# Optimization experiments

Measured on AMD Instinct MI355X. Metric: run time of the kernel, lower is better.

The kernel has to match this reference:

```python
import jax, jax.numpy as jnp
import numpy as np

N_HEADS = 8
N_GROUPS = 8  # n_channels=256 > 64
COLOR_WEIGHT = 1.2
EPS = 1e-5


def setup_inputs() -> dict:
    key = jax.random.key(0)
    ks = jax.random.split(key, 6)
    B, C, H, W = 16, 256, 32, 32
    x = jax.random.normal(ks[0], (B, C, H, W), dtype=jnp.float32)
    std = 0.02
    wq = jax.random.normal(ks[1], (C, C), dtype=jnp.float32) * std
    wk = jax.random.normal(ks[2], (C, C), dtype=jnp.float32) * std
    wv = jax.random.normal(ks[3], (C, C), dtype=jnp.float32) * std
    wo = jax.random.normal(ks[4], (C, C), dtype=jnp.float32) * std
    bq = jnp.zeros((C,), jnp.float32)
    bk = jnp.zeros((C,), jnp.float32)
    bv = jnp.zeros((C,), jnp.float32)
    bo = jnp.zeros((C,), jnp.float32)
    gn_w = jnp.ones((C,), jnp.float32)
    gn_b = jnp.zeros((C,), jnp.float32)
    return {"x": x, "wq": wq, "bq": bq, "wk": wk, "bk": bk,
            "wv": wv, "bv": bv, "wo": wo, "bo": bo,
            "gn_w": gn_w, "gn_b": gn_b}


def reference(x, wq, bq, wk, bk, wv, bv, wo, bo, gn_w, gn_b):
    B, C, H, W = x.shape
    S = H * W
    nh = N_HEADS
    hd = C // nh
    scale = hd ** (-0.5)

    # GroupNorm over (channels_per_group, spatial) per sample
    xf = x.reshape(B, C, S)
    xg = xf.reshape(B, N_GROUPS, (C // N_GROUPS) * S)
    mean = xg.mean(axis=-1, keepdims=True)
    var = xg.var(axis=-1, keepdims=True)
    xn = ((xg - mean) * jax.lax.rsqrt(var + EPS)).reshape(B, C, S)
    xn = xn * gn_w[None, :, None] + gn_b[None, :, None]

    xt = jnp.swapaxes(xn, 1, 2)  # [B, S, C]
    q = xt @ wq.T + bq
    k = xt @ wk.T + bk
    v = xt @ wv.T + bv
    # [B, S, C] -> [B, nh, S, hd]
    q = q.reshape(B, S, nh, hd).transpose(0, 2, 1, 3)
    k = k.reshape(B, S, nh, hd).transpose(0, 2, 1, 3)
    v = v.reshape(B, S, nh, hd).transpose(0, 2, 1, 3)

    attn = jnp.einsum('bhid,bhjd->bhij', q, k) * scale  # [B, nh, S, S]
    # color bias (is_grayscale=False path): k.transpose(-2,-1).reshape(B,nh,S,hd)
    k_color = jnp.swapaxes(k, -2, -1).reshape(B, nh, S, hd)
    color_attn = jnp.abs(q - k_color).mean(axis=-1, keepdims=True)  # [B,nh,S,1]
    attn = attn + COLOR_WEIGHT * color_attn
    attn = jax.nn.softmax(attn, axis=-1)
    # dropout is inference no-op

    out = jnp.einsum('bhij,bhjd->bhid', attn, v)  # [B, nh, S, hd]
    out = out.transpose(0, 2, 1, 3).reshape(B, S, C)
    out = out @ wo.T + bo
    out = jnp.swapaxes(out, 1, 2).reshape(B, C, H, W)
    return out
```

## Files before the change

### kernel.cpp

```cpp
#include <hip/hip_runtime.h>


typedef __attribute__((ext_vector_type(8))) short bf16x8;
typedef __attribute__((ext_vector_type(4))) float f32x4;

static __device__ __forceinline__ unsigned cvt_pk(float lo, float hi) {
  unsigned r;
  asm("v_cvt_pk_bf16_f32 %0, %1, %2" : "=v"(r) : "v"(lo), "v"(hi));
  return r;
}

__global__ __launch_bounds__(256) void prep_kernel(
    const float* __restrict__ x, float2* __restrict__ stats,
    const float* __restrict__ w0, const float* __restrict__ w1,
    const float* __restrict__ w2, const float* __restrict__ w3,
    short* __restrict__ o0, short* __restrict__ o1,
    short* __restrict__ o2, short* __restrict__ o3) {
  int tid = threadIdx.x;
  if (blockIdx.x < 128) {
    __shared__ float red[8];
    int bg = blockIdx.x;
    const float4* x4 = (const float4*)(x + (size_t)bg * 32 * 1024);
    float s = 0.f, ss = 0.f;
    for (int i = tid; i < 8192; i += 256) {
      float4 vv = x4[i];
      s += (vv.x + vv.y) + (vv.z + vv.w);
      ss += vv.x * vv.x + vv.y * vv.y + vv.z * vv.z + vv.w * vv.w;
    }
#pragma unroll
    for (int o = 32; o > 0; o >>= 1) {
      s += __shfl_down(s, o);
      ss += __shfl_down(ss, o);
    }
    if ((tid & 63) == 0) { red[tid >> 6] = s; red[4 + (tid >> 6)] = ss; }
    __syncthreads();
    if (tid == 0) {
      float S = (red[0] + red[1]) + (red[2] + red[3]);
      float SS = (red[4] + red[5]) + (red[6] + red[7]);
      float mean = S * (1.f / 32768.f);
      float var = SS * (1.f / 32768.f) - mean * mean;
      stats[bg] = make_float2(mean, rsqrtf(var + 1e-5f));
    }
  } else {
    int idx = blockIdx.x - 128;
    int sel = idx >> 5, blk = idx & 31;
    const float* src = sel == 0 ? w0 : sel == 1 ? w1 : sel == 2 ? w2 : w3;
    short* dst = sel == 0 ? o0 : sel == 1 ? o1 : sel == 2 ? o2 : o3;
    int i = (blk * 256 + tid) * 8;
    float4 a = *(const float4*)(src + i);
    float4 b = *(const float4*)(src + i + 4);
    uint4 r;
    r.x = cvt_pk(a.x, a.y);
    r.y = cvt_pk(a.z, a.w);
    r.z = cvt_pk(b.x, b.y);
    r.w = cvt_pk(b.z, b.w);
    *(uint4*)(dst + i) = r;
  }
}

__global__ __launch_bounds__(256, 4) void qkv_mfma(
    const float* __restrict__ x, const float2* __restrict__ stats,
    const float* __restrict__ gnw, const float* __restrict__ gnb,
    const short* __restrict__ Wq, const short* __restrict__ Wk,
    const short* __restrict__ Wv,
    const float* __restrict__ bq, const float* __restrict__ bk,
    const float* __restrict__ bv, short* __restrict__ outq,
    short* __restrict__ outk, short* __restrict__ outvt, float scaleq) {
  __shared__ __align__(16) char smem[20480];
  short* As = (short*)smem;
  int tid = threadIdx.x;
  int m0 = blockIdx.x * 64, n0 = blockIdx.y * 64;
  int w = tid >> 6, lane = tid & 63, g = lane >> 4, c = lane & 15;
  int wm = w >> 1, wn = w & 1;
  int srow = tid >> 2, sk = (tid & 3) * 8;
  int bsmp = m0 >> 10, s0 = m0 & 1023;
  int c2 = tid & 15, sg = tid >> 4;
  const float4* xb = (const float4*)(x + (size_t)(bsmp * 256) * 1024);
  unsigned* A32 = (unsigned*)As;
  f32x4 accq[2][2], acck[2][2], accv[2][2];
#pragma unroll
  for (int i = 0; i < 2; ++i)
#pragma unroll
    for (int j = 0; j < 2; ++j) {
      accq[i][j] = (f32x4){0.f, 0.f, 0.f, 0.f};
      acck[i][j] = (f32x4){0.f, 0.f, 0.f, 0.f};
      accv[i][j] = (f32x4){0.f, 0.f, 0.f, 0.f};
    }
  for (int kb = 0; kb < 8; ++kb) {
    float2 st = stats[bsmp * 8 + kb];
    int ch0 = kb * 32 + c2 * 2;
    float a0 = gnw[ch0] * st.y, b0v = gnb[ch0] - st.x * a0;
    float a1 = gnw[ch0 + 1] * st.y, b1v = gnb[ch0 + 1] - st.x * a1;
    float4 u = xb[(size_t)ch0 * 256 + (s0 >> 2) + sg];
    float4 v = xb[(size_t)(ch0 + 1) * 256 + (s0 >> 2) + sg];
    __syncthreads();
    {
      int r0 = (sg * 4) * 20 + c2;
      A32[r0]      = cvt_pk(u.x * a0 + b0v, v.x * a1 + b1v);
      A32[r0 + 20] = cvt_pk(u.y * a0 + b0v, v.y * a1 + b1v);
      A32[r0 + 40] = cvt_pk(u.z * a0 + b0v, v.z * a1 + b1v);
      A32[r0 + 60] = cvt_pk(u.w * a0 + b0v, v.w * a1 + b1v);
    }
    *(bf16x8*)(As + 2560 + srow * 40 + sk) =
        *(const bf16x8*)(Wq + (size_t)(n0 + srow) * 256 + kb * 32 + sk);
    *(bf16x8*)(As + 5120 + srow * 40 + sk) =
        *(const bf16x8*)(Wk + (size_t)(n0 + srow) * 256 + kb * 32 + sk);
    *(bf16x8*)(As + 7680 + srow * 40 + sk) =
        *(const bf16x8*)(Wv + (size_t)(n0 + srow) * 256 + kb * 32 + sk);
    __syncthreads();
    bf16x8 af[2], wfq[2], wfk[2], wfv[2];
#pragma unroll
    for (int i = 0; i < 2; ++i)
      af[i] = *(const bf16x8*)(As + (wm * 32 + i * 16 + c) * 40 + g * 8);
#pragma unroll
    for (int j = 0; j < 2; ++j) {
      int rr = (wn * 32 + j * 16 + c) * 40 + g * 8;
      wfq[j] = *(const bf16x8*)(As + 2560 + rr);
      wfk[j] = *(const bf16x8*)(As + 5120 + rr);
      wfv[j] = *(const bf16x8*)(As + 7680 + rr);
    }
#pragma unroll
    for (int i = 0; i < 2; ++i)
#pragma unroll
      for (int j = 0; j < 2; ++j) {
        accq[i][j] = __builtin_amdgcn_mfma_f32_16x16x32_bf16(wfq[j], af[i], accq[i][j], 0, 0, 0);
        acck[i][j] = __builtin_amdgcn_mfma_f32_16x16x32_bf16(wfk[j], af[i], acck[i][j], 0, 0, 0);
        accv[i][j] = __builtin_amdgcn_mfma_f32_16x16x32_bf16(af[i], wfv[j], accv[i][j], 0, 0, 0);
      }
  }
  __syncthreads();
  short* Tb = (short*)smem;
  int mrd = tid >> 2, ncol = (tid & 3) * 16;
#pragma unroll
  for (int i = 0; i < 2; ++i)
#pragma unroll
    for (int j = 0; j < 2; ++j) {
      float4 b4 = *(const float4*)&bq[n0 + wn * 32 + j * 16 + 4 * g];
      float v0 = (accq[i][j][0] + b4.x) * scaleq;
      float v1 = (accq[i][j][1] + b4.y) * scaleq;
      float v2 = (accq[i][j][2] + b4.z) * scaleq;
      float v3 = (accq[i][j][3] + b4.w) * scaleq;
      *(uint2*)(Tb + (wm * 32 + i * 16 + c) * 72 + wn * 32 + j * 16 + 4 * g) =
          make_uint2(cvt_pk(v0, v1), cvt_pk(v2, v3));
    }
  __syncthreads();
  {
    bf16x8 r0 = *(const bf16x8*)(Tb + mrd * 72 + ncol);
    bf16x8 r1 = *(const bf16x8*)(Tb + mrd * 72 + ncol + 8);
    short* dst = outq + (size_t)(m0 + mrd) * 256 + n0 + ncol;
    *(bf16x8*)dst = r0;
    *(bf16x8*)(dst + 8) = r1;
  }
  __syncthreads();
#pragma unroll
  for (int i = 0; i < 2; ++i)
#pragma unroll
    for (int j = 0; j < 2; ++j) {
      float4 b4 = *(const float4*)&bk[n0 + wn * 32 + j * 16 + 4 * g];
      float v0 = acck[i][j][0] + b4.x;
      float v1 = acck[i][j][1] + b4.y;
      float v2 = acck[i][j][2] + b4.z;
      float v3 = acck[i][j][3] + b4.w;
      *(uint2*)(Tb + (wm * 32 + i * 16 + c) * 72 + wn * 32 + j * 16 + 4 * g) =
          make_uint2(cvt_pk(v0, v1), cvt_pk(v2, v3));
    }
  __syncthreads();
  {
    bf16x8 r0 = *(const bf16x8*)(Tb + mrd * 72 + ncol);
    bf16x8 r1 = *(const bf16x8*)(Tb + mrd * 72 + ncol + 8);
    short* dst = outk + (size_t)(m0 + mrd) * 256 + n0 + ncol;
    *(bf16x8*)dst = r0;
    *(bf16x8*)(dst + 8) = r1;
  }
  __syncthreads();
#pragma unroll
  for (int i = 0; i < 2; ++i)
#pragma unroll
    for (int j = 0; j < 2; ++j) {
      float bvv = bv[n0 + wn * 32 + j * 16 + c];
      float v0 = accv[i][j][0] + bvv;
      float v1 = accv[i][j][1] + bvv;
      float v2 = accv[i][j][2] + bvv;
      float v3 = accv[i][j][3] + bvv;
      *(uint2*)(Tb + (wn * 32 + j * 16 + c) * 72 + wm * 32 + i * 16 + 4 * g) =
          make_uint2(cvt_pk(v0, v1), cvt_pk(v2, v3));
    }
  __syncthreads();
  {
    bf16x8 r0 = *(const bf16x8*)(Tb + mrd * 72 + ncol);
    bf16x8 r1 = *(const bf16x8*)(Tb + mrd * 72 + ncol + 8);
    short* dst = outvt + (size_t)(bsmp * 256 + n0 + mrd) * 1024 + s0 + ncol;
    *(bf16x8*)dst = r0;
    *(bf16x8*)(dst + 8) = r1;
  }
}

#define KSTR 40
#define VSTR 72
#define PSTR 72

__global__ __launch_bounds__(256, 4) void flash_mfma(
    const short* __restrict__ q, const short* __restrict__ k,
    const short* __restrict__ vt, short* __restrict__ out) {
  __shared__ short Ks[2][64 * KSTR];
  __shared__ short Vts[2][32 * VSTR];
  __shared__ short Ps[4 * 32 * PSTR];
  int id = blockIdx.x;
  int swz = (id & 7) * 128 + (id >> 3);
  int bh = swz >> 3, qt = swz & 7;
  int b = bh >> 3, h = bh & 7;
  int tid = threadIdx.x;
  int w = tid >> 6, lane = tid & 63, g = lane >> 4, c = lane & 15;
  short* Psw = Ps + w * 32 * PSTR;
  const size_t qrow0 = (size_t)b * 1024 + qt * 128 + w * 32;
  const int hoff = h * 32;
  bf16x8 aq[2];
#pragma unroll
  for (int mt = 0; mt < 2; ++mt)
    aq[mt] = *(const bf16x8*)(q + (qrow0 + mt * 16 + c) * 256 + hoff + g * 8);
  bf16x8 ones;
#pragma unroll
  for (int i = 0; i < 8; ++i) ones[i] = (short)0x3F80;
  f32x4 o_acc[2][2], accl[2];
#pragma unroll
  for (int mt = 0; mt < 2; ++mt) {
    accl[mt] = (f32x4){0.f, 0.f, 0.f, 0.f};
#pragma unroll
    for (int nt = 0; nt < 2; ++nt) o_acc[mt][nt] = (f32x4){0.f, 0.f, 0.f, 0.f};
  }
  const int kr = tid >> 2, kch = (tid & 3) * 8;
  const int vr = tid >> 3, vch = (tid & 7) * 8;
  const short* kbase = k + ((size_t)b * 1024) * 256 + hoff;
  const short* vbase = vt + (((size_t)b * 8 + h) * 32) * 1024;
  {
    bf16x8 k0 = *(const bf16x8*)(kbase + (size_t)kr * 256 + kch);
    bf16x8 v0 = *(const bf16x8*)(vbase + (size_t)vr * 1024 + vch);
    *(bf16x8*)(&Ks[0][kr * KSTR + kch]) = k0;
    *(bf16x8*)(&Vts[0][vr * VSTR + vch]) = v0;
  }
  __syncthreads();
  int cur = 0;
#pragma unroll 2
  for (int t = 0; t < 16; ++t) {
    bf16x8 kN, vN;
    if (t < 15) {
      kN = *(const bf16x8*)(kbase + (size_t)((t + 1) * 64 + kr) * 256 + kch);
      vN = *(const bf16x8*)(vbase + (size_t)vr * 1024 + (t + 1) * 64 + vch);
    }
    bf16x8 bk4[4];
#pragma unroll
    for (int kt = 0; kt < 4; ++kt)
      bk4[kt] = *(const bf16x8*)(&Ks[cur][(kt * 16 + c) * KSTR + g * 8]);
    f32x4 sc[2][4];
#pragma unroll
    for (int mt = 0; mt < 2; ++mt)
#pragma unroll
      for (int kt = 0; kt < 4; ++kt)
        sc[mt][kt] = __builtin_amdgcn_mfma_f32_16x16x32_bf16(
            bk4[kt], aq[mt], (f32x4){0.f, 0.f, 0.f, 0.f}, 0, 0, 0);
#pragma unroll
    for (int mt = 0; mt < 2; ++mt)
#pragma unroll
      for (int kt = 0; kt < 4; ++kt) {
        float p0 = __builtin_amdgcn_exp2f(sc[mt][kt][0]);
        float p1 = __builtin_amdgcn_exp2f(sc[mt][kt][1]);
        float p2 = __builtin_amdgcn_exp2f(sc[mt][kt][2]);
        float p3 = __builtin_amdgcn_exp2f(sc[mt][kt][3]);
        *(uint2*)(Psw + (mt * 16 + c) * PSTR + kt * 16 + 4 * g) =
            make_uint2(cvt_pk(p0, p1), cvt_pk(p2, p3));
      }
#pragma unroll
    for (int jt = 0; jt < 2; ++jt) {
      bf16x8 av[2], bp[2];
#pragma unroll
      for (int nt = 0; nt < 2; ++nt)
        av[nt] = *(const bf16x8*)(&Vts[cur][(nt * 16 + c) * VSTR + jt * 32 + g * 8]);
#pragma unroll
      for (int mt = 0; mt < 2; ++mt)
        bp[mt] = *(const bf16x8*)(Psw + (mt * 16 + c) * PSTR + jt * 32 + g * 8);
#pragma unroll
      for (int mt = 0; mt < 2; ++mt) {
#pragma unroll
        for (int nt = 0; nt < 2; ++nt)
          o_acc[mt][nt] = __builtin_amdgcn_mfma_f32_16x16x32_bf16(
              av[nt], bp[mt], o_acc[mt][nt], 0, 0, 0);
        accl[mt] = __builtin_amdgcn_mfma_f32_16x16x32_bf16(ones, bp[mt], accl[mt], 0, 0, 0);
      }
    }
    if (t < 15) {
      *(bf16x8*)(&Ks[cur ^ 1][kr * KSTR + kch]) = kN;
      *(bf16x8*)(&Vts[cur ^ 1][vr * VSTR + vch]) = vN;
      __syncthreads();
      cur ^= 1;
    }
  }
#pragma unroll
  for (int mt = 0; mt < 2; ++mt) {
    float linv = 1.0f / accl[mt][0];
#pragma unroll
    for (int nt = 0; nt < 2; ++nt) {
      float v0 = o_acc[mt][nt][0] * linv;
      float v1 = o_acc[mt][nt][1] * linv;
      float v2 = o_acc[mt][nt][2] * linv;
      float v3 = o_acc[mt][nt][3] * linv;
      *(uint2*)(out + (qrow0 + mt * 16 + c) * 256 + hoff + nt * 16 + 4 * g) =
          make_uint2(cvt_pk(v0, v1), cvt_pk(v2, v3));
    }
  }
}

__global__ __launch_bounds__(256) void gemm_out(
    const short* __restrict__ A, const short* __restrict__ W,
    const float* __restrict__ bias, float* __restrict__ out) {
  __shared__ __align__(16) char smem[10240];
  short* As = (short*)smem;
  short* Ws = (short*)(smem + 5120);
  int tid = threadIdx.x;
  int m0 = blockIdx.y * 64, n0 = blockIdx.x * 64;
  int w = tid >> 6, lane = tid & 63, g = lane >> 4, c = lane & 15;
  int wm = w >> 1, wn = w & 1;
  int srow = tid >> 2, sk = (tid & 3) * 8;
  f32x4 acc[2][2];
#pragma unroll
  for (int i = 0; i < 2; ++i)
#pragma unroll
    for (int j = 0; j < 2; ++j) acc[i][j] = (f32x4){0.f, 0.f, 0.f, 0.f};
  for (int kb = 0; kb < 8; ++kb) {
    __syncthreads();
    *(bf16x8*)(As + srow * 40 + sk) =
        *(const bf16x8*)(A + (size_t)(m0 + srow) * 256 + kb * 32 + sk);
    *(bf16x8*)(Ws + srow * 40 + sk) =
        *(const bf16x8*)(W + (size_t)(n0 + srow) * 256 + kb * 32 + sk);
    __syncthreads();
    bf16x8 af[2], wf[2];
#pragma unroll
    for (int i = 0; i < 2; ++i)
      af[i] = *(const bf16x8*)(As + (wm * 32 + i * 16 + c) * 40 + g * 8);
#pragma unroll
    for (int j = 0; j < 2; ++j)
      wf[j] = *(const bf16x8*)(Ws + (wn * 32 + j * 16 + c) * 40 + g * 8);
#pragma unroll
    for (int i = 0; i < 2; ++i)
#pragma unroll
      for (int j = 0; j < 2; ++j)
        acc[i][j] = __builtin_amdgcn_mfma_f32_16x16x32_bf16(af[i], wf[j], acc[i][j], 0, 0, 0);
  }
  int bsmp = m0 >> 10, s0 = m0 & 1023;
  float* Tf = (float*)smem;
  for (int half = 0; half < 2; ++half) {
    __syncthreads();
    if (wn == half) {
#pragma unroll
      for (int j = 0; j < 2; ++j) {
        float bvh = bias[n0 + half * 32 + j * 16 + c];
        int nl = j * 16 + c;
#pragma unroll
        for (int i = 0; i < 2; ++i)
#pragma unroll
          for (int r = 0; r < 4; ++r)
            Tf[nl * 68 + ((wm * 32 + i * 16 + 4 * g + r) ^ ((nl & 7) << 2))] =
                acc[i][j][r] + bvh;
      }
    }
    __syncthreads();
    int n = tid >> 3, mc = (tid & 7) * 8;
    float4 v0 = *(const float4*)(Tf + n * 68 + ((mc + 0) ^ ((n & 7) << 2)));
    float4 v1 = *(const float4*)(Tf + n * 68 + ((mc + 4) ^ ((n & 7) << 2)));
    float* dst = out + ((size_t)(bsmp * 256) + n0 + half * 32 + n) * 1024 + s0 + mc;
    *(float4*)dst = v0;
    *(float4*)(dst + 4) = v1;
  }
}

extern "C" void kernel_launch(void* const* d_in, const int* in_sizes, int n_in,
                              void* d_out, int out_size, void* d_ws, size_t ws_size,
                              hipStream_t stream) {
  const float* x   = (const float*)d_in[0];
  const float* wq  = (const float*)d_in[1];
  const float* bq  = (const float*)d_in[2];
  const float* wk  = (const float*)d_in[3];
  const float* bk  = (const float*)d_in[4];
  const float* wv  = (const float*)d_in[5];
  const float* bv  = (const float*)d_in[6];
  const float* wo  = (const float*)d_in[7];
  const float* bo  = (const float*)d_in[8];
  const float* gnw = (const float*)d_in[9];
  const float* gnb = (const float*)d_in[10];
  float* out = (float*)d_out;

  const size_t NE = (size_t)16 * 1024 * 256;
  short* sw  = (short*)d_ws;
  float2* stats = (float2*)sw;
  short* qb  = sw + NE;
  short* kb  = sw + 2 * NE;
  short* vtb = sw + 3 * NE;
  short* ao  = sw + 4 * NE;
  short* wqb = sw + 5 * NE;
  short* wkb = wqb + 65536;
  short* wvb = wkb + 65536;
  short* wob = wvb + 65536;

  const float SCALE_Q = (float)(0.17677669529663689 * 1.4426950408889634);
  dim3 blk(256);
  prep_kernel<<<dim3(256), blk, 0, stream>>>(x, stats, wq, wk, wv, wo,
                                             wqb, wkb, wvb, wob);
  qkv_mfma<<<dim3(256, 4), blk, 0, stream>>>(x, stats, gnw, gnb, wqb, wkb, wvb,
                                             bq, bk, bv, qb, kb, vtb, SCALE_Q);
  flash_mfma<<<dim3(1024), blk, 0, stream>>>(qb, kb, vtb, ao);
  gemm_out<<<dim3(4, 256), blk, 0, stream>>>(ao, wob, bo, out);
}
```

Measured before the change: 79.67 us.

## Double M-tile to 128 rows in QKV and output projection GEMMs

Both the fused GroupNorm+QKV GEMM and the output projection GEMM now compute 128x64 tiles per block instead of 64x64, with each warp holding 4x2 MFMA accumulators. This halves the number of blocks and the re-reading of the weight tiles per output row, and widens the epilogue stores. The gemm_out grid order is also swapped so that consecutive blocks walk along M. In exchange, register pressure rises (qkv launch bounds drop to 2 blocks per SM), occupancy falls, and only 512 blocks remain to spread across the CUs.

Result: slower. 83.00 us (+4.2%).

```diff
diff --git a/kernel.cpp b/kernel.cpp
--- a/kernel.cpp
+++ b/kernel.cpp
@@ -58,7 +58,7 @@
   }
 }
 
-__global__ __launch_bounds__(256, 4) void qkv_mfma(
+__global__ __launch_bounds__(256, 2) void qkv_mfma(
     const float* __restrict__ x, const float2* __restrict__ stats,
     const float* __restrict__ gnw, const float* __restrict__ gnb,
     const short* __restrict__ Wq, const short* __restrict__ Wk,
@@ -66,20 +66,20 @@
     const float* __restrict__ bq, const float* __restrict__ bk,
     const float* __restrict__ bv, short* __restrict__ outq,
     short* __restrict__ outk, short* __restrict__ outvt, float scaleq) {
-  __shared__ __align__(16) char smem[20480];
+  __shared__ __align__(16) char smem[25600];
   short* As = (short*)smem;
   int tid = threadIdx.x;
-  int m0 = blockIdx.x * 64, n0 = blockIdx.y * 64;
+  int m0 = blockIdx.x * 128, n0 = blockIdx.y * 64;
   int w = tid >> 6, lane = tid & 63, g = lane >> 4, c = lane & 15;
   int wm = w >> 1, wn = w & 1;
   int srow = tid >> 2, sk = (tid & 3) * 8;
   int bsmp = m0 >> 10, s0 = m0 & 1023;
-  int c2 = tid & 15, sg = tid >> 4;
+  int c2 = tid & 15, sgb = tid >> 4;
   const float4* xb = (const float4*)(x + (size_t)(bsmp * 256) * 1024);
   unsigned* A32 = (unsigned*)As;
-  f32x4 accq[2][2], acck[2][2], accv[2][2];
-#pragma unroll
-  for (int i = 0; i < 2; ++i)
+  f32x4 accq[4][2], acck[4][2], accv[4][2];
+#pragma unroll
+  for (int i = 0; i < 4; ++i)
 #pragma unroll
     for (int j = 0; j < 2; ++j) {
       accq[i][j] = (f32x4){0.f, 0.f, 0.f, 0.f};
@@ -91,36 +91,43 @@
     int ch0 = kb * 32 + c2 * 2;
     float a0 = gnw[ch0] * st.y, b0v = gnb[ch0] - st.x * a0;
     float a1 = gnw[ch0 + 1] * st.y, b1v = gnb[ch0 + 1] - st.x * a1;
-    float4 u = xb[(size_t)ch0 * 256 + (s0 >> 2) + sg];
-    float4 v = xb[(size_t)(ch0 + 1) * 256 + (s0 >> 2) + sg];
+    float4 u0 = xb[(size_t)ch0 * 256 + (s0 >> 2) + sgb];
+    float4 v0 = xb[(size_t)(ch0 + 1) * 256 + (s0 >> 2) + sgb];
+    float4 u1 = xb[(size_t)ch0 * 256 + (s0 >> 2) + sgb + 16];
+    float4 v1 = xb[(size_t)(ch0 + 1) * 256 + (s0 >> 2) + sgb + 16];
     __syncthreads();
     {
-      int r0 = (sg * 4) * 20 + c2;
-      A32[r0]      = cvt_pk(u.x * a0 + b0v, v.x * a1 + b1v);
-      A32[r0 + 20] = cvt_pk(u.y * a0 + b0v, v.y * a1 + b1v);
-      A32[r0 + 40] = cvt_pk(u.z * a0 + b0v, v.z * a1 + b1v);
-      A32[r0 + 60] = cvt_pk(u.w * a0 + b0v, v.w * a1 + b1v);
-    }
-    *(bf16x8*)(As + 2560 + srow * 40 + sk) =
+      int r0 = (sgb * 4) * 20 + c2;
+      A32[r0]      = cvt_pk(u0.x * a0 + b0v, v0.x * a1 + b1v);
+      A32[r0 + 20] = cvt_pk(u0.y * a0 + b0v, v0.y * a1 + b1v);
+      A32[r0 + 40] = cvt_pk(u0.z * a0 + b0v, v0.z * a1 + b1v);
+      A32[r0 + 60] = cvt_pk(u0.w * a0 + b0v, v0.w * a1 + b1v);
+      int r1 = ((sgb + 16) * 4) * 20 + c2;
+      A32[r1]      = cvt_pk(u1.x * a0 + b0v, v1.x * a1 + b1v);
+      A32[r1 + 20] = cvt_pk(u1.y * a0 + b0v, v1.y * a1 + b1v);
+      A32[r1 + 40] = cvt_pk(u1.z * a0 + b0v, v1.z * a1 + b1v);
+      A32[r1 + 60] = cvt_pk(u1.w * a0 + b0v, v1.w * a1 + b1v);
+    }
+    *(bf16x8*)(As + 5120 + srow * 40 + sk) =
         *(const bf16x8*)(Wq + (size_t)(n0 + srow) * 256 + kb * 32 + sk);
-    *(bf16x8*)(As + 5120 + srow * 40 + sk) =
+    *(bf16x8*)(As + 7680 + srow * 40 + sk) =
         *(const bf16x8*)(Wk + (size_t)(n0 + srow) * 256 + kb * 32 + sk);
-    *(bf16x8*)(As + 7680 + srow * 40 + sk) =
+    *(bf16x8*)(As + 10240 + srow * 40 + sk) =
         *(const bf16x8*)(Wv + (size_t)(n0 + srow) * 256 + kb * 32 + sk);
     __syncthreads();
-    bf16x8 af[2], wfq[2], wfk[2], wfv[2];
-#pragma unroll
-    for (int i = 0; i < 2; ++i)
-      af[i] = *(const bf16x8*)(As + (wm * 32 + i * 16 + c) * 40 + g * 8);
+    bf16x8 af[4], wfq[2], wfk[2], wfv[2];
+#pragma unroll
+    for (int i = 0; i < 4; ++i)
+      af[i] = *(const bf16x8*)(As + (wm * 64 + i * 16 + c) * 40 + g * 8);
 #pragma unroll
     for (int j = 0; j < 2; ++j) {
       int rr = (wn * 32 + j * 16 + c) * 40 + g * 8;
-      wfq[j] = *(const bf16x8*)(As + 2560 + rr);
-      wfk[j] = *(const bf16x8*)(As + 5120 + rr);
-      wfv[j] = *(const bf16x8*)(As + 7680 + rr);
-    }
-#pragma unroll
-    for (int i = 0; i < 2; ++i)
+      wfq[j] = *(const bf16x8*)(As + 5120 + rr);
+      wfk[j] = *(const bf16x8*)(As + 7680 + rr);
+      wfv[j] = *(const bf16x8*)(As + 10240 + rr);
+    }
+#pragma unroll
+    for (int i = 0; i < 4; ++i)
 #pragma unroll
       for (int j = 0; j < 2; ++j) {
         accq[i][j] = __builtin_amdgcn_mfma_f32_16x16x32_bf16(wfq[j], af[i], accq[i][j], 0, 0, 0);
@@ -130,9 +137,9 @@
   }
   __syncthreads();
   short* Tb = (short*)smem;
-  int mrd = tid >> 2, ncol = (tid & 3) * 16;
-#pragma unroll
-  for (int i = 0; i < 2; ++i)
+  int mrd = tid >> 1, ncol = (tid & 1) * 32;
+#pragma unroll
+  for (int i = 0; i < 4; ++i)
 #pragma unroll
     for (int j = 0; j < 2; ++j) {
       float4 b4 = *(const float4*)&bq[n0 + wn * 32 + j * 16 + 4 * g];
@@ -140,20 +147,21 @@
       float v1 = (accq[i][j][1] + b4.y) * scaleq;
       float v2 = (accq[i][j][2] + b4.z) * scaleq;
       float v3 = (accq[i][j][3] + b4.w) * scaleq;
-      *(uint2*)(Tb + (wm * 32 + i * 16 + c) * 72 + wn * 32 + j * 16 + 4 * g) =
+      *(uint2*)(Tb + (wm * 64 + i * 16 + c) * 72 + wn * 32 + j * 16 + 4 * g) =
           make_uint2(cvt_pk(v0, v1), cvt_pk(v2, v3));
     }
   __syncthreads();
   {
-    bf16x8 r0 = *(const bf16x8*)(Tb + mrd * 72 + ncol);
-    bf16x8 r1 = *(const bf16x8*)(Tb + mrd * 72 + ncol + 8);
     short* dst = outq + (size_t)(m0 + mrd) * 256 + n0 + ncol;
-    *(bf16x8*)dst = r0;
-    *(bf16x8*)(dst + 8) = r1;
-  }
-  __syncthreads();
-#pragma unroll
-  for (int i = 0; i < 2; ++i)
+    const short* src = Tb + mrd * 72 + ncol;
+    *(bf16x8*)(dst)      = *(const bf16x8*)(src);
+    *(bf16x8*)(dst + 8)  = *(const bf16x8*)(src + 8);
+    *(bf16x8*)(dst + 16) = *(const bf16x8*)(src + 16);
+    *(bf16x8*)(dst + 24) = *(const bf16x8*)(src + 24);
+  }
+  __syncthreads();
+#pragma unroll
+  for (int i = 0; i < 4; ++i)
 #pragma unroll
     for (int j = 0; j < 2; ++j) {
       float4 b4 = *(const float4*)&bk[n0 + wn * 32 + j * 16 + 4 * g];
@@ -161,20 +169,21 @@
       float v1 = acck[i][j][1] + b4.y;
       float v2 = acck[i][j][2] + b4.z;
       float v3 = acck[i][j][3] + b4.w;
-      *(uint2*)(Tb + (wm * 32 + i * 16 + c) * 72 + wn * 32 + j * 16 + 4 * g) =
+      *(uint2*)(Tb + (wm * 64 + i * 16 + c) * 72 + wn * 32 + j * 16 + 4 * g) =
           make_uint2(cvt_pk(v0, v1), cvt_pk(v2, v3));
     }
   __syncthreads();
   {
-    bf16x8 r0 = *(const bf16x8*)(Tb + mrd * 72 + ncol);
-    bf16x8 r1 = *(const bf16x8*)(Tb + mrd * 72 + ncol + 8);
     short* dst = outk + (size_t)(m0 + mrd) * 256 + n0 + ncol;
-    *(bf16x8*)dst = r0;
-    *(bf16x8*)(dst + 8) = r1;
-  }
-  __syncthreads();
-#pragma unroll
-  for (int i = 0; i < 2; ++i)
+    const short* src = Tb + mrd * 72 + ncol;
+    *(bf16x8*)(dst)      = *(const bf16x8*)(src);
+    *(bf16x8*)(dst + 8)  = *(const bf16x8*)(src + 8);
+    *(bf16x8*)(dst + 16) = *(const bf16x8*)(src + 16);
+    *(bf16x8*)(dst + 24) = *(const bf16x8*)(src + 24);
+  }
+  __syncthreads();
+#pragma unroll
+  for (int i = 0; i < 4; ++i)
 #pragma unroll
     for (int j = 0; j < 2; ++j) {
       float bvv = bv[n0 + wn * 32 + j * 16 + c];
@@ -182,16 +191,18 @@
       float v1 = accv[i][j][1] + bvv;
       float v2 = accv[i][j][2] + bvv;
       float v3 = accv[i][j][3] + bvv;
-      *(uint2*)(Tb + (wn * 32 + j * 16 + c) * 72 + wm * 32 + i * 16 + 4 * g) =
+      *(uint2*)(Tb + (wn * 32 + j * 16 + c) * 136 + wm * 64 + i * 16 + 4 * g) =
           make_uint2(cvt_pk(v0, v1), cvt_pk(v2, v3));
     }
   __syncthreads();
   {
-    bf16x8 r0 = *(const bf16x8*)(Tb + mrd * 72 + ncol);
-    bf16x8 r1 = *(const bf16x8*)(Tb + mrd * 72 + ncol + 8);
-    short* dst = outvt + (size_t)(bsmp * 256 + n0 + mrd) * 1024 + s0 + ncol;
-    *(bf16x8*)dst = r0;
-    *(bf16x8*)(dst + 8) = r1;
+    int vr = tid >> 2, vc = (tid & 3) * 32;
+    short* dst = outvt + ((size_t)(bsmp * 256) + n0 + vr) * 1024 + s0 + vc;
+    const short* src = Tb + vr * 136 + vc;
+    *(bf16x8*)(dst)      = *(const bf16x8*)(src);
+    *(bf16x8*)(dst + 8)  = *(const bf16x8*)(src + 8);
+    *(bf16x8*)(dst + 16) = *(const bf16x8*)(src + 16);
+    *(bf16x8*)(dst + 24) = *(const bf16x8*)(src + 24);
   }
 }
 
@@ -309,38 +320,42 @@
   }
 }
 
-__global__ __launch_bounds__(256) void gemm_out(
+__global__ __launch_bounds__(256, 4) void gemm_out(
     const short* __restrict__ A, const short* __restrict__ W,
     const float* __restrict__ bias, float* __restrict__ out) {
-  __shared__ __align__(16) char smem[10240];
+  __shared__ __align__(16) char smem[17408];
   short* As = (short*)smem;
-  short* Ws = (short*)(smem + 5120);
+  short* Ws = (short*)(smem + 10240);
   int tid = threadIdx.x;
-  int m0 = blockIdx.y * 64, n0 = blockIdx.x * 64;
+  int m0 = blockIdx.x * 128, n0 = blockIdx.y * 64;
   int w = tid >> 6, lane = tid & 63, g = lane >> 4, c = lane & 15;
   int wm = w >> 1, wn = w & 1;
+  int arow = tid >> 1, ak = (tid & 1) * 16;
   int srow = tid >> 2, sk = (tid & 3) * 8;
-  f32x4 acc[2][2];
-#pragma unroll
-  for (int i = 0; i < 2; ++i)
+  f32x4 acc[4][2];
+#pragma unroll
+  for (int i = 0; i < 4; ++i)
 #pragma unroll
     for (int j = 0; j < 2; ++j) acc[i][j] = (f32x4){0.f, 0.f, 0.f, 0.f};
   for (int kb = 0; kb < 8; ++kb) {
     __syncthreads();
-    *(bf16x8*)(As + srow * 40 + sk) =
-        *(const bf16x8*)(A + (size_t)(m0 + srow) * 256 + kb * 32 + sk);
+    {
+      const short* srcA = A + (size_t)(m0 + arow) * 256 + kb * 32 + ak;
+      *(bf16x8*)(As + arow * 40 + ak)     = *(const bf16x8*)(srcA);
+      *(bf16x8*)(As + arow * 40 + ak + 8) = *(const bf16x8*)(srcA + 8);
+    }
     *(bf16x8*)(Ws + srow * 40 + sk) =
         *(const bf16x8*)(W + (size_t)(n0 + srow) * 256 + kb * 32 + sk);
     __syncthreads();
-    bf16x8 af[2], wf[2];
-#pragma unroll
-    for (int i = 0; i < 2; ++i)
-      af[i] = *(const bf16x8*)(As + (wm * 32 + i * 16 + c) * 40 + g * 8);
+    bf16x8 af[4], wf[2];
+#pragma unroll
+    for (int i = 0; i < 4; ++i)
+      af[i] = *(const bf16x8*)(As + (wm * 64 + i * 16 + c) * 40 + g * 8);
 #pragma unroll
     for (int j = 0; j < 2; ++j)
       wf[j] = *(const bf16x8*)(Ws + (wn * 32 + j * 16 + c) * 40 + g * 8);
 #pragma unroll
-    for (int i = 0; i < 2; ++i)
+    for (int i = 0; i < 4; ++i)
 #pragma unroll
       for (int j = 0; j < 2; ++j)
         acc[i][j] = __builtin_amdgcn_mfma_f32_16x16x32_bf16(af[i], wf[j], acc[i][j], 0, 0, 0);
@@ -355,20 +370,25 @@
         float bvh = bias[n0 + half * 32 + j * 16 + c];
         int nl = j * 16 + c;
 #pragma unroll
-        for (int i = 0; i < 2; ++i)
+        for (int i = 0; i < 4; ++i)
 #pragma unroll
           for (int r = 0; r < 4; ++r)
-            Tf[nl * 68 + ((wm * 32 + i * 16 + 4 * g + r) ^ ((nl & 7) << 2))] =
+            Tf[nl * 132 + ((wm * 64 + i * 16 + 4 * g + r) ^ ((nl & 7) << 2))] =
                 acc[i][j][r] + bvh;
       }
     }
     __syncthreads();
-    int n = tid >> 3, mc = (tid & 7) * 8;
-    float4 v0 = *(const float4*)(Tf + n * 68 + ((mc + 0) ^ ((n & 7) << 2)));
-    float4 v1 = *(const float4*)(Tf + n * 68 + ((mc + 4) ^ ((n & 7) << 2)));
+    int n = tid >> 3, mc = (tid & 7) * 16;
+    int sw = (n & 7) << 2;
+    float4 v0 = *(const float4*)(Tf + n * 132 + ((mc + 0) ^ sw));
+    float4 v1 = *(const float4*)(Tf + n * 132 + ((mc + 4) ^ sw));
+    float4 v2 = *(const float4*)(Tf + n * 132 + ((mc + 8) ^ sw));
+    float4 v3 = *(const float4*)(Tf + n * 132 + ((mc + 12) ^ sw));
     float* dst = out + ((size_t)(bsmp * 256) + n0 + half * 32 + n) * 1024 + s0 + mc;
     *(float4*)dst = v0;
     *(float4*)(dst + 4) = v1;
+    *(float4*)(dst + 8) = v2;
+    *(float4*)(dst + 12) = v3;
   }
 }
 
@@ -404,8 +424,8 @@
   dim3 blk(256);
   prep_kernel<<<dim3(256), blk, 0, stream>>>(x, stats, wq, wk, wv, wo,
                                              wqb, wkb, wvb, wob);
-  qkv_mfma<<<dim3(256, 4), blk, 0, stream>>>(x, stats, gnw, gnb, wqb, wkb, wvb,
+  qkv_mfma<<<dim3(128, 4), blk, 0, stream>>>(x, stats, gnw, gnb, wqb, wkb, wvb,
                                              bq, bk, bv, qb, kb, vtb, SCALE_Q);
   flash_mfma<<<dim3(1024), blk, 0, stream>>>(qb, kb, vtb, ao);
-  gemm_out<<<dim3(4, 256), blk, 0, stream>>>(ao, wob, bo, out);
-}
+  gemm_out<<<dim3(128, 4), blk, 0, stream>>>(ao, wob, bo, out);
+}
```
